# Kernel optimization log

Hardware: AMD Instinct MI355X
Metric: run time of the kernel (lower is better)

Reference implementation:

```python
import jax, jax.numpy as jnp
import numpy as np

NUM_HEADS = 16
FUTURE_FRAMES = 2
DIM = 1024


def setup_inputs() -> dict:
    key = jax.random.key(0)
    kx, kqkv, kp, kb = jax.random.split(key, 4)
    B, T = 2, 2048
    x = jax.random.normal(kx, (B, T, DIM), dtype=jnp.float32)
    # torch Linear weights stored transposed for direct x @ W use
    w_qkv = jax.random.normal(kqkv, (DIM, 3 * DIM), dtype=jnp.float32) * (DIM ** -0.5)
    w_proj = jax.random.normal(kp, (DIM, DIM), dtype=jnp.float32) * (DIM ** -0.5)
    b_proj = jax.random.normal(kb, (DIM,), dtype=jnp.float32) * 0.01
    return {"x": x, "w_qkv": w_qkv, "w_proj": w_proj, "b_proj": b_proj}


def reference(x, w_qkv, w_proj, b_proj):
    B, T, dim = x.shape
    H = NUM_HEADS
    hd = dim // H
    qkv = x @ w_qkv                                    # (B, T, 3*dim)
    q, k, v = jnp.split(qkv, 3, axis=-1)
    # (B, H, T, hd)
    q = q.reshape(B, T, H, hd).transpose(0, 2, 1, 3)
    k = k.reshape(B, T, H, hd).transpose(0, 2, 1, 3)
    v = v.reshape(B, T, H, hd).transpose(0, 2, 1, 3)
    scale = hd ** -0.5
    scores = jnp.einsum('bhqd,bhkd->bhqk', q, k) * scale
    # banded mask: query i may attend keys j with i <= j <= i + future_frames
    i = jnp.arange(T)[:, None]
    j = jnp.arange(T)[None, :]
    allowed = (j >= i) & (j <= i + FUTURE_FRAMES)       # (T, T)
    scores = jnp.where(allowed[None, None], scores, -jnp.inf)
    attn = jax.nn.softmax(scores, axis=-1)
    out = jnp.einsum('bhqk,bhkd->bhqd', attn, v)        # (B, H, T, hd)
    out = out.transpose(0, 2, 1, 3).reshape(B, T, dim)
    return out @ w_proj + b_proj
```

## Files before the change

### kernel.cpp

```cpp
#include <hip/hip_runtime.h>
#include <hip/hip_bf16.h>
#include <cstdint>
#include <cstddef>

#define T_SEQ 2048
#define NBATCH 2
#define DIMSZ 1024
#define NHEAD 16
#define HDIM 64

typedef float f32x4 __attribute__((ext_vector_type(4)));
typedef short bf16x8 __attribute__((ext_vector_type(8)));

__device__ __forceinline__ void gld_lds16(const __hip_bfloat16* g, __hip_bfloat16* l) {
    __builtin_amdgcn_global_load_lds(
        (const __attribute__((address_space(1))) unsigned int*)g,
        (__attribute__((address_space(3))) unsigned int*)l,
        16, 0, 0);
}

__device__ __forceinline__ float bf2f(unsigned short u) {
    union { unsigned int i; float f; } c; c.i = (unsigned int)u << 16; return c.f;
}

__global__ __launch_bounds__(256) void prep(
    const float* __restrict__ x,      __hip_bfloat16* __restrict__ xb,
    const float* __restrict__ wqkv,   __hip_bfloat16* __restrict__ wqkvT,
    const float* __restrict__ wproj,  __hip_bfloat16* __restrict__ wprojT)
{
    __shared__ float tile[64][65];
    const int b = blockIdx.x;
    if (b < 4096) {
        int i = (b * 256 + threadIdx.x) * 4;
        float4 v = *(const float4*)(x + i);
        union { __hip_bfloat16 h[4]; ushort4 u; } pk;
        pk.h[0] = __hip_bfloat16(v.x); pk.h[1] = __hip_bfloat16(v.y);
        pk.h[2] = __hip_bfloat16(v.z); pk.h[3] = __hip_bfloat16(v.w);
        *(ushort4*)(xb + i) = pk.u;
        return;
    }
    const float* in; __hip_bfloat16* out; int C, c0, r0;
    if (b < 4864) {
        int bb = b - 4096; in = wqkv; out = wqkvT; C = 3072;
        c0 = (bb % 48) * 64; r0 = (bb / 48) * 64;
    } else {
        int bb = b - 4864; in = wproj; out = wprojT; C = 1024;
        c0 = (bb & 15) * 64; r0 = (bb >> 4) * 64;
    }
    const int tx = threadIdx.x & 63, ty = threadIdx.x >> 6;
#pragma unroll
    for (int p = 0; p < 16; ++p) {
        int row = ty + p * 4;
        tile[row][tx] = in[(size_t)(r0 + row) * C + c0 + tx];
    }
    __syncthreads();
#pragma unroll
    for (int p = 0; p < 16; ++p) {
        int orow = ty + p * 4;
        out[(size_t)(c0 + orow) * 1024 + r0 + tx] = __hip_bfloat16(tile[tx][orow]);
    }
}

__global__ __launch_bounds__(256) void gemm_bt_128(
    const __hip_bfloat16* __restrict__ A,
    const __hip_bfloat16* __restrict__ Bt,
    __hip_bfloat16* __restrict__ C,
    int M, int N, int K)
{
    __shared__ __align__(16) __hip_bfloat16 As[2 * 128 * 32];
    __shared__ __align__(16) __hip_bfloat16 Bs[2 * 128 * 32];

    const int tid  = threadIdx.x;
    const int wv   = tid >> 6;
    const int lane = tid & 63;
    const int bn   = blockIdx.x, bm = blockIdx.y;
    const int wm   = wv >> 1, wn = wv & 1;

    f32x4 acc[4][4] = {};

    const int srow = lane >> 2;
    const int scol = (lane & 3) * 8;

    const __hip_bfloat16* Ag = A  + (size_t)(bm * 128) * K;
    const __hip_bfloat16* Bg = Bt + (size_t)(bn * 128) * K;

    const int fm = lane & 15;
    const int fq = (lane >> 4) * 8;

    for (int kk = 0; kk < K; kk += 64) {
#pragma unroll
        for (int kh = 0; kh < 2; ++kh)
#pragma unroll
            for (int it = 0; it < 2; ++it) {
                int row = (it * 4 + wv) * 16 + srow;
                gld_lds16(Ag + (size_t)row * K + kk + kh * 32 + scol,
                          As + kh * 4096 + row * 32 + scol);
                gld_lds16(Bg + (size_t)row * K + kk + kh * 32 + scol,
                          Bs + kh * 4096 + row * 32 + scol);
            }
        __syncthreads();

#pragma unroll
        for (int kh = 0; kh < 2; ++kh) {
            bf16x8 af[4], bfr[4];
#pragma unroll
            for (int i = 0; i < 4; ++i)
                af[i] = *(const bf16x8*)(As + kh * 4096 + (wm * 64 + i * 16 + fm) * 32 + fq);
#pragma unroll
            for (int j = 0; j < 4; ++j)
                bfr[j] = *(const bf16x8*)(Bs + kh * 4096 + (wn * 64 + j * 16 + fm) * 32 + fq);
#pragma unroll
            for (int i = 0; i < 4; ++i)
#pragma unroll
                for (int j = 0; j < 4; ++j)
                    acc[i][j] = __builtin_amdgcn_mfma_f32_16x16x32_bf16(af[i], bfr[j], acc[i][j], 0, 0, 0);
        }
        __syncthreads();
    }

    const int fcol  = lane & 15;
    const int frow4 = (lane >> 4) * 4;
    const int cm0 = bm * 128 + wm * 64;
    const int cn0 = bn * 128 + wn * 64;
#pragma unroll
    for (int j = 0; j < 4; ++j) {
        int col = cn0 + j * 16 + fcol;
#pragma unroll
        for (int i = 0; i < 4; ++i)
#pragma unroll
            for (int r = 0; r < 4; ++r) {
                int row = cm0 + i * 16 + frow4 + r;
                C[(size_t)row * N + col] = __hip_bfloat16(acc[i][j][r]);
            }
    }
}

__global__ __launch_bounds__(256, 2) void gemm_bt_64(
    const __hip_bfloat16* __restrict__ A,
    const __hip_bfloat16* __restrict__ Bt,
    const float* __restrict__ bias,
    float* __restrict__ C,
    int M, int N, int K)
{
    __shared__ __align__(16) __hip_bfloat16 As2[4 * 64 * 32];
    __shared__ __align__(16) __hip_bfloat16 Bs2[4 * 128 * 32];

    const int tid  = threadIdx.x;
    const int wv   = tid >> 6;
    const int lane = tid & 63;
    const int bn   = blockIdx.x, bm = blockIdx.y;
    const int wm   = wv >> 1, wn = wv & 1;

    f32x4 acc[2][4] = {};

    const int srow = lane >> 2;
    const int scol = (lane & 3) * 8;

    const __hip_bfloat16* Ag = A  + (size_t)(bm * 64) * K;
    const __hip_bfloat16* Bg = Bt + (size_t)(bn * 128) * K;

    const int fm = lane & 15;
    const int fq = (lane >> 4) * 8;

    for (int kk = 0; kk < K; kk += 128) {
#pragma unroll
        for (int kh = 0; kh < 4; ++kh) {
            {
                int row = wv * 16 + srow;
                gld_lds16(Ag + (size_t)row * K + kk + kh * 32 + scol,
                          As2 + kh * 2048 + row * 32 + scol);
            }
#pragma unroll
            for (int it = 0; it < 2; ++it) {
                int row = (it * 4 + wv) * 16 + srow;
                gld_lds16(Bg + (size_t)row * K + kk + kh * 32 + scol,
                          Bs2 + kh * 4096 + row * 32 + scol);
            }
        }
        __syncthreads();

#pragma unroll
        for (int kh = 0; kh < 4; ++kh) {
            bf16x8 af[2], bfr[4];
#pragma unroll
            for (int i = 0; i < 2; ++i)
                af[i] = *(const bf16x8*)(As2 + kh * 2048 + (wm * 32 + i * 16 + fm) * 32 + fq);
#pragma unroll
            for (int j = 0; j < 4; ++j)
                bfr[j] = *(const bf16x8*)(Bs2 + kh * 4096 + (wn * 64 + j * 16 + fm) * 32 + fq);
#pragma unroll
            for (int i = 0; i < 2; ++i)
#pragma unroll
                for (int j = 0; j < 4; ++j)
                    acc[i][j] = __builtin_amdgcn_mfma_f32_16x16x32_bf16(af[i], bfr[j], acc[i][j], 0, 0, 0);
        }
        __syncthreads();
    }

    const int fcol  = lane & 15;
    const int frow4 = (lane >> 4) * 4;
    const int cm0 = bm * 64 + wm * 32;
    const int cn0 = bn * 128 + wn * 64;
#pragma unroll
    for (int j = 0; j < 4; ++j) {
        int col = cn0 + j * 16 + fcol;
        float bv = bias[col];
#pragma unroll
        for (int i = 0; i < 2; ++i)
#pragma unroll
            for (int r = 0; r < 4; ++r) {
                int row = cm0 + i * 16 + frow4 + r;
                C[(size_t)row * N + col] = acc[i][j][r] + bv;
            }
    }
}

__global__ __launch_bounds__(256) void attn_banded(
    const __hip_bfloat16* __restrict__ qkv,
    __hip_bfloat16* __restrict__ o)
{
    const int tid = threadIdx.x;
    const int t8  = tid & 127;
    const int r   = blockIdx.x * 2 + (tid >> 7);
    const int t   = r & (T_SEQ - 1);
    const size_t rb = (size_t)r * (3 * DIMSZ);
    const int d0 = t8 * 8;

    bf16x8 qu = *(const bf16x8*)(qkv + rb + d0);
    float q[8];
#pragma unroll
    for (int i = 0; i < 8; ++i) q[i] = bf2f((unsigned short)qu[i]);

    float s[3], vv[3][8];
#pragma unroll
    for (int j = 0; j < 3; ++j) {
        bool ok = (t + j) < T_SEQ;
        size_t rbj = ok ? rb + (size_t)j * (3 * DIMSZ) : rb;
        bf16x8 ku = *(const bf16x8*)(qkv + rbj + DIMSZ + d0);
        bf16x8 vu = *(const bf16x8*)(qkv + rbj + 2 * DIMSZ + d0);
        float d = 0.f;
#pragma unroll
        for (int i = 0; i < 8; ++i) {
            vv[j][i] = bf2f((unsigned short)vu[i]);
            d += q[i] * bf2f((unsigned short)ku[i]);
        }
        d += __shfl_xor(d, 4, 64);
        d += __shfl_xor(d, 2, 64);
        d += __shfl_xor(d, 1, 64);
        s[j] = ok ? d * 0.125f : -1e30f;
    }
    float m  = fmaxf(s[0], fmaxf(s[1], s[2]));
    float p0 = __expf(s[0] - m), p1 = __expf(s[1] - m), p2 = __expf(s[2] - m);
    float inv = 1.0f / (p0 + p1 + p2);
    union { __hip_bfloat16 h[8]; bf16x8 u; } pk;
#pragma unroll
    for (int i = 0; i < 8; ++i)
        pk.h[i] = __hip_bfloat16((p0 * vv[0][i] + p1 * vv[1][i] + p2 * vv[2][i]) * inv);
    *(bf16x8*)(o + (size_t)r * DIMSZ + d0) = pk.u;
}

extern "C" void kernel_launch(void* const* d_in, const int* in_sizes, int n_in,
                              void* d_out, int out_size, void* d_ws, size_t ws_size,
                              hipStream_t stream) {
    const float* x      = (const float*)d_in[0];
    const float* w_qkv  = (const float*)d_in[1];
    const float* w_proj = (const float*)d_in[2];
    const float* b_proj = (const float*)d_in[3];
    float* out = (float*)d_out;

    const int M = NBATCH * T_SEQ;

    char* ws = (char*)d_ws;
    __hip_bfloat16* xb     = (__hip_bfloat16*)(ws);
    __hip_bfloat16* attn   = (__hip_bfloat16*)(ws);
    __hip_bfloat16* wqkvT  = (__hip_bfloat16*)(ws + (8u  << 20));
    __hip_bfloat16* wprojT = (__hip_bfloat16*)(ws + (14u << 20));
    __hip_bfloat16* qkv    = (__hip_bfloat16*)(ws + (16u << 20));

    prep<<<5120, 256, 0, stream>>>(x, xb, w_qkv, wqkvT, w_proj, wprojT);

    gemm_bt_128<<<dim3(3 * DIMSZ / 128, M / 128), 256, 0, stream>>>(
        xb, wqkvT, qkv, M, 3 * DIMSZ, DIMSZ);

    attn_banded<<<M / 2, 256, 0, stream>>>(qkv, attn);

    gemm_bt_64<<<dim3(DIMSZ / 128, M / 64), 256, 0, stream>>>(
        attn, wprojT, b_proj, out, M, DIMSZ, DIMSZ);
}
```

Baseline: 141.4 us.

## Fuse banded attention into output projection GEMM A-tile producer

Removes the standalone banded-attention kernel and computes the attention output on the fly inside the projection GEMM, writing each 64x128 A slice directly to shared memory. This avoids writing and re-reading the intermediate attention buffer and drops one kernel launch. In exchange, each of the eight column blocks recomputes attention for its rows, multiplying q/k/v reads from the qkv buffer. The block grows to 512 threads with smaller per-wave tiles.

```diff
diff --git a/kernel.cpp b/kernel.cpp
--- a/kernel.cpp
+++ b/kernel.cpp
@@ -135,63 +135,119 @@
     }
 }
 
-__global__ __launch_bounds__(256, 2) void gemm_bt_64(
-    const __hip_bfloat16* __restrict__ A,
+__global__ __launch_bounds__(512) void attn_gemm2(
+    const __hip_bfloat16* __restrict__ qkv,
     const __hip_bfloat16* __restrict__ Bt,
     const float* __restrict__ bias,
-    float* __restrict__ C,
-    int M, int N, int K)
+    float* __restrict__ C)
 {
-    __shared__ __align__(16) __hip_bfloat16 As2[4 * 64 * 32];
-    __shared__ __align__(16) __hip_bfloat16 Bs2[4 * 128 * 32];
+    __shared__ __align__(16) __hip_bfloat16 As2[4][64][32];
+    __shared__ __align__(16) __hip_bfloat16 Bs2[4][128][32];
 
     const int tid  = threadIdx.x;
     const int wv   = tid >> 6;
     const int lane = tid & 63;
-    const int bn   = blockIdx.x, bm = blockIdx.y;
-    const int wm   = wv >> 1, wn = wv & 1;
-
-    f32x4 acc[2][4] = {};
-
-    const int srow = lane >> 2;
-    const int scol = (lane & 3) * 8;
-
-    const __hip_bfloat16* Ag = A  + (size_t)(bm * 64) * K;
-    const __hip_bfloat16* Bg = Bt + (size_t)(bn * 128) * K;
+    const int bn   = blockIdx.x;
+    const int bm   = blockIdx.y;
+    const int wm   = wv >> 2, wn = wv & 3;
+
+    const int arow = tid >> 3;
+    const int g8   = tid & 7;
+    const int r    = bm * 64 + arow;
+    const int t    = r & (T_SEQ - 1);
+    const __hip_bfloat16* qrow = qkv + (size_t)r * (3 * DIMSZ);
+
+    const int srow = tid >> 2;
+    const int scol = (tid & 3) * 8;
+
+    const __hip_bfloat16* Bg = Bt + (size_t)(bn * 128) * DIMSZ;
 
     const int fm = lane & 15;
     const int fq = (lane >> 4) * 8;
 
-    for (int kk = 0; kk < K; kk += 128) {
+    f32x4 acc[2][2] = {};
+
+    const bool ok1 = (t + 1) < T_SEQ;
+    const bool ok2 = (t + 2) < T_SEQ;
+    const size_t roff1 = ok1 ? (size_t)(3 * DIMSZ) : 0;
+    const size_t roff2 = ok2 ? (size_t)(6 * DIMSZ) : 0;
+
+    for (int kk = 0; kk < DIMSZ; kk += 128) {
+#pragma unroll
+        for (int kh = 0; kh < 4; ++kh)
+            gld_lds16(Bg + (size_t)srow * DIMSZ + kk + kh * 32 + scol,
+                      &Bs2[kh][srow][scol]);
+
+        const int d0 = kk + g8 * 16;
+        bf16x8 qa = *(const bf16x8*)(qrow + d0);
+        bf16x8 qb = *(const bf16x8*)(qrow + d0 + 8);
+        bf16x8 ka[3], kb[3], va[3], vb[3];
+        {
+            const __hip_bfloat16* k0 = qrow + DIMSZ + d0;
+            const __hip_bfloat16* v0 = qrow + 2 * DIMSZ + d0;
+            ka[0] = *(const bf16x8*)(k0);            kb[0] = *(const bf16x8*)(k0 + 8);
+            va[0] = *(const bf16x8*)(v0);            vb[0] = *(const bf16x8*)(v0 + 8);
+            ka[1] = *(const bf16x8*)(k0 + roff1);    kb[1] = *(const bf16x8*)(k0 + roff1 + 8);
+            va[1] = *(const bf16x8*)(v0 + roff1);    vb[1] = *(const bf16x8*)(v0 + roff1 + 8);
+            ka[2] = *(const bf16x8*)(k0 + roff2);    kb[2] = *(const bf16x8*)(k0 + roff2 + 8);
+            va[2] = *(const bf16x8*)(v0 + roff2);    vb[2] = *(const bf16x8*)(v0 + roff2 + 8);
+        }
+        float qf[16];
+#pragma unroll
+        for (int i = 0; i < 8; ++i) {
+            qf[i]     = bf2f((unsigned short)qa[i]);
+            qf[i + 8] = bf2f((unsigned short)qb[i]);
+        }
+        float s[3];
+#pragma unroll
+        for (int j = 0; j < 3; ++j) {
+            float d = 0.f;
+#pragma unroll
+            for (int i = 0; i < 8; ++i) {
+                d += qf[i]     * bf2f((unsigned short)ka[j][i]);
+                d += qf[i + 8] * bf2f((unsigned short)kb[j][i]);
+            }
+            d += __shfl_xor(d, 1, 64);
+            d += __shfl_xor(d, 2, 64);
+            s[j] = d * 0.125f;
+        }
+        if (!ok1) s[1] = -1e30f;
+        if (!ok2) s[2] = -1e30f;
+        float m  = fmaxf(s[0], fmaxf(s[1], s[2]));
+        float p0 = __expf(s[0] - m), p1 = __expf(s[1] - m), p2 = __expf(s[2] - m);
+        float inv = 1.0f / (p0 + p1 + p2);
+        union { __hip_bfloat16 h[8]; bf16x8 u; } w0, w1;
+#pragma unroll
+        for (int i = 0; i < 8; ++i) {
+            float oa = p0 * bf2f((unsigned short)va[0][i])
+                     + p1 * bf2f((unsigned short)va[1][i])
+                     + p2 * bf2f((unsigned short)va[2][i]);
+            float ob = p0 * bf2f((unsigned short)vb[0][i])
+                     + p1 * bf2f((unsigned short)vb[1][i])
+                     + p2 * bf2f((unsigned short)vb[2][i]);
+            w0.h[i] = __hip_bfloat16(oa * inv);
+            w1.h[i] = __hip_bfloat16(ob * inv);
+        }
+        {
+            const int kh = g8 >> 1, c0 = (g8 & 1) * 16;
+            *(bf16x8*)&As2[kh][arow][c0]     = w0.u;
+            *(bf16x8*)&As2[kh][arow][c0 + 8] = w1.u;
+        }
+        __syncthreads();
+
 #pragma unroll
         for (int kh = 0; kh < 4; ++kh) {
-            {
-                int row = wv * 16 + srow;
-                gld_lds16(Ag + (size_t)row * K + kk + kh * 32 + scol,
-                          As2 + kh * 2048 + row * 32 + scol);
-            }
-#pragma unroll
-            for (int it = 0; it < 2; ++it) {
-                int row = (it * 4 + wv) * 16 + srow;
-                gld_lds16(Bg + (size_t)row * K + kk + kh * 32 + scol,
-                          Bs2 + kh * 4096 + row * 32 + scol);
-            }
-        }
-        __syncthreads();
-
-#pragma unroll
-        for (int kh = 0; kh < 4; ++kh) {
-            bf16x8 af[2], bfr[4];
+            bf16x8 af[2], bfr[2];
 #pragma unroll
             for (int i = 0; i < 2; ++i)
-                af[i] = *(const bf16x8*)(As2 + kh * 2048 + (wm * 32 + i * 16 + fm) * 32 + fq);
-#pragma unroll
-            for (int j = 0; j < 4; ++j)
-                bfr[j] = *(const bf16x8*)(Bs2 + kh * 4096 + (wn * 64 + j * 16 + fm) * 32 + fq);
+                af[i] = *(const bf16x8*)&As2[kh][wm * 32 + i * 16 + fm][fq];
+#pragma unroll
+            for (int j = 0; j < 2; ++j)
+                bfr[j] = *(const bf16x8*)&Bs2[kh][wn * 32 + j * 16 + fm][fq];
 #pragma unroll
             for (int i = 0; i < 2; ++i)
 #pragma unroll
-                for (int j = 0; j < 4; ++j)
+                for (int j = 0; j < 2; ++j)
                     acc[i][j] = __builtin_amdgcn_mfma_f32_16x16x32_bf16(af[i], bfr[j], acc[i][j], 0, 0, 0);
         }
         __syncthreads();
@@ -200,63 +256,19 @@
     const int fcol  = lane & 15;
     const int frow4 = (lane >> 4) * 4;
     const int cm0 = bm * 64 + wm * 32;
-    const int cn0 = bn * 128 + wn * 64;
-#pragma unroll
-    for (int j = 0; j < 4; ++j) {
+    const int cn0 = bn * 128 + wn * 32;
+#pragma unroll
+    for (int j = 0; j < 2; ++j) {
         int col = cn0 + j * 16 + fcol;
         float bv = bias[col];
 #pragma unroll
         for (int i = 0; i < 2; ++i)
 #pragma unroll
-            for (int r = 0; r < 4; ++r) {
-                int row = cm0 + i * 16 + frow4 + r;
-                C[(size_t)row * N + col] = acc[i][j][r] + bv;
-            }
-    }
-}
-
-__global__ __launch_bounds__(256) void attn_banded(
-    const __hip_bfloat16* __restrict__ qkv,
-    __hip_bfloat16* __restrict__ o)
-{
-    const int tid = threadIdx.x;
-    const int t8  = tid & 127;
-    const int r   = blockIdx.x * 2 + (tid >> 7);
-    const int t   = r & (T_SEQ - 1);
-    const size_t rb = (size_t)r * (3 * DIMSZ);
-    const int d0 = t8 * 8;
-
-    bf16x8 qu = *(const bf16x8*)(qkv + rb + d0);
-    float q[8];
-#pragma unroll
-    for (int i = 0; i < 8; ++i) q[i] = bf2f((unsigned short)qu[i]);
-
-    float s[3], vv[3][8];
-#pragma unroll
-    for (int j = 0; j < 3; ++j) {
-        bool ok = (t + j) < T_SEQ;
-        size_t rbj = ok ? rb + (size_t)j * (3 * DIMSZ) : rb;
-        bf16x8 ku = *(const bf16x8*)(qkv + rbj + DIMSZ + d0);
-        bf16x8 vu = *(const bf16x8*)(qkv + rbj + 2 * DIMSZ + d0);
-        float d = 0.f;
-#pragma unroll
-        for (int i = 0; i < 8; ++i) {
-            vv[j][i] = bf2f((unsigned short)vu[i]);
-            d += q[i] * bf2f((unsigned short)ku[i]);
-        }
-        d += __shfl_xor(d, 4, 64);
-        d += __shfl_xor(d, 2, 64);
-        d += __shfl_xor(d, 1, 64);
-        s[j] = ok ? d * 0.125f : -1e30f;
-    }
-    float m  = fmaxf(s[0], fmaxf(s[1], s[2]));
-    float p0 = __expf(s[0] - m), p1 = __expf(s[1] - m), p2 = __expf(s[2] - m);
-    float inv = 1.0f / (p0 + p1 + p2);
-    union { __hip_bfloat16 h[8]; bf16x8 u; } pk;
-#pragma unroll
-    for (int i = 0; i < 8; ++i)
-        pk.h[i] = __hip_bfloat16((p0 * vv[0][i] + p1 * vv[1][i] + p2 * vv[2][i]) * inv);
-    *(bf16x8*)(o + (size_t)r * DIMSZ + d0) = pk.u;
+            for (int rr = 0; rr < 4; ++rr) {
+                int row = cm0 + i * 16 + frow4 + rr;
+                C[(size_t)row * DIMSZ + col] = acc[i][j][rr] + bv;
+            }
+    }
 }
 
 extern "C" void kernel_launch(void* const* d_in, const int* in_sizes, int n_in,
@@ -272,7 +284,6 @@
 
     char* ws = (char*)d_ws;
     __hip_bfloat16* xb     = (__hip_bfloat16*)(ws);
-    __hip_bfloat16* attn   = (__hip_bfloat16*)(ws);
     __hip_bfloat16* wqkvT  = (__hip_bfloat16*)(ws + (8u  << 20));
     __hip_bfloat16* wprojT = (__hip_bfloat16*)(ws + (14u << 20));
     __hip_bfloat16* qkv    = (__hip_bfloat16*)(ws + (16u << 20));
@@ -282,8 +293,6 @@
     gemm_bt_128<<<dim3(3 * DIMSZ / 128, M / 128), 256, 0, stream>>>(
         xb, wqkvT, qkv, M, 3 * DIMSZ, DIMSZ);
 
-    attn_banded<<<M / 2, 256, 0, stream>>>(qkv, attn);
-
-    gemm_bt_64<<<dim3(DIMSZ / 128, M / 64), 256, 0, stream>>>(
-        attn, wprojT, b_proj, out, M, DIMSZ, DIMSZ);
-}
+    attn_gemm2<<<dim3(DIMSZ / 128, M / 64), 512, 0, stream>>>(
+        qkv, wprojT, b_proj, out);
+}
```

Measured after the change: 154.0 us. 1.09x slower.
